# Kernel optimization log

Measured on AMD Instinct MI355X. Metric: run time of the kernel, lower is better.

The kernel has to match this reference:

```python
import jax, jax.numpy as jnp
import numpy as np

CUTOFF = 0.05

def _freq_filter(x_chw, filter_type):
    # x_chw: [C,H,W] = batch element 0, detached in the original (stop_gradient)
    x = jax.lax.stop_gradient(x_chw)
    C, H, W = x.shape
    a = jnp.abs(x)
    mn = a.min(axis=(1, 2), keepdims=True)
    ptp = a.max(axis=(1, 2), keepdims=True) - mn
    # np.uint8(255*(a-mn)/ptp): values in [0,255], cast truncates -> floor
    q = jnp.floor(255.0 * (a - mn) / ptp)
    f = jnp.fft.fftshift(jnp.fft.fft2(q), axes=(-2, -1))
    crow, ccol = H // 2, W // 2
    dr, dc = int(CUTOFF * crow), int(CUTOFF * ccol)
    m = jnp.zeros((H, W), dtype=q.dtype)
    m = m.at[crow - dr:crow + dr, ccol - dc:ccol + dc].set(1.0)
    if filter_type == 'low_pass':
        m = 1.0 - m  # note: original 'low_pass' actually removes low freqs
    out = jnp.abs(jnp.fft.ifft2(jnp.fft.ifftshift(f * m, axes=(-2, -1))))
    return out.astype(x_chw.dtype)  # [C,H,W]

def _conv1x1(x, w, b):
    # x: [B,C,H,W], w: [O,C], b: [O]
    return jnp.einsum('oc,bchw->bohw', w, x) + b[None, :, None, None]

def setup_inputs() -> dict:
    key = jax.random.key(0)
    ks = jax.random.split(key, 7)
    B, C, H, W = 1, 256, 96, 96
    fuse = jax.random.normal(ks[0], (B, C, H, W), dtype=jnp.float32)
    s = 1.0 / np.sqrt(C)
    Wq = jax.random.normal(ks[1], (C, C), dtype=jnp.float32) * s
    bq = jax.random.normal(ks[2], (C,), dtype=jnp.float32) * 0.01
    Wk = jax.random.normal(ks[3], (C, C), dtype=jnp.float32) * s
    bk = jax.random.normal(ks[4], (C,), dtype=jnp.float32) * 0.01
    Wv = jax.random.normal(ks[5], (C, C), dtype=jnp.float32) * s
    bv = jax.random.normal(ks[6], (C,), dtype=jnp.float32) * 0.01
    return {"fuse": fuse, "Wq": Wq, "bq": bq, "Wk": Wk, "bk": bk, "Wv": Wv, "bv": bv}

def reference(fuse, Wq, bq, Wk, bk, Wv, bv):
    B, C, H, W = fuse.shape
    scale = 1.0 / (C ** 0.5)
    # frequency-filtered maps (computed from batch 0, broadcast to all batches)
    FQ = jnp.broadcast_to(_freq_filter(fuse[0], 'high_pass'), fuse.shape)
    FK = jnp.broadcast_to(_freq_filter(fuse[0], 'low_pass'), fuse.shape)
    fuse_Query = _conv1x1(FQ, Wq, bq).reshape(B, C, H * W)     # [B,C,HW]
    fuse_Q_mask = fuse_Query.reshape(B * H, C * W)             # [B*H, C*W]
    fuse_Query_t = jnp.transpose(fuse_Query, (0, 2, 1))        # [B,HW,C]
    fuse_Key = _conv1x1(FK, Wk, bk).reshape(B, C, H * W)       # [B,C,HW]
    Fuse_Q_mask = jnp.max(fuse_Q_mask, axis=0, keepdims=True)  # [1, C*W]
    mask_KQ = jnp.einsum('bnc,bcm->bnm', fuse_Query_t, fuse_Key) * scale  # [B,HW,HW]
    mask_KQ = jax.nn.softmax(mask_KQ, axis=0)  # softmax over batch dim (as in original)
    mask_KQ = jnp.max(mask_KQ, axis=1)                         # [B,HW]
    mask_KQ = mask_KQ.reshape(-1, W)                           # [B*H, W]
    mask_KQ = jnp.max(mask_KQ, axis=-1, keepdims=True)         # [B*H, 1]
    mask = (mask_KQ @ Fuse_Q_mask).reshape(B, C, H, W)
    fuse_Value = _conv1x1(fuse, Wv, bv)
    return fuse_Value + fuse_Value * mask
```

## Files before the change

kernel.cpp:

```cpp
#include <hip/hip_runtime.h>
#include <math.h>

#define CCH 256
#define HW  9216
#define CW  24576
#define TWO_PI 6.28318530717958647692f

typedef __attribute__((ext_vector_type(8))) short short8;
typedef __attribute__((ext_vector_type(4))) float f32x4;

__device__ inline unsigned short f2bf(float f) {
    unsigned u = __float_as_uint(f);
    unsigned r = (u + 0x7FFFu + ((u >> 16) & 1u)) >> 16;
    return (unsigned short)r;
}

__global__ __launch_bounds__(768) void k_pre(const float* __restrict__ x,
                                             const float* __restrict__ Wq,
                                             const float* __restrict__ Wv,
                                             short8* __restrict__ Wqt,
                                             short8* __restrict__ Wvt,
                                             unsigned* __restrict__ FQm,
                                             float* __restrict__ Fg) {
    __shared__ float qa[HW];
    __shared__ float cs[96][2];
    __shared__ float Gp[8][96][5];
    __shared__ float Gs[96][6];
    __shared__ float red[24];
    __shared__ float s_mn, s_ptp;
    int bid = blockIdx.x, t = threadIdx.x;

    if (bid >= 256) {
        int widx = bid - 256;
        if (t < 256) {
            const float* src = (widx >= 32) ? Wv : Wq;
            short8* dst = (widx >= 32) ? Wvt : Wqt;
            int cidx = (widx & 31) * 256 + t;
            int ot = cidx >> 11, kc = (cidx >> 6) & 31, m = cidx & 63;
            const float* s = src + (ot * 64 + m) * 256 + kc * 8;
            short8 v;
            #pragma unroll
            for (int e = 0; e < 8; ++e) v[e] = (short)f2bf(s[e]);
            dst[cidx] = v;
        }
        return;
    }

    int c = bid;
    if (t < 96) FQm[c * 96 + t] = 0u;
    const float* xp = x + c * HW;
    if (t < 96) { float a = TWO_PI * (float)t / 96.0f; cs[t][0] = cosf(a); cs[t][1] = sinf(a); }
    float lo = 1e30f, hi = 0.f;
    #pragma unroll
    for (int i = 0; i < 12; ++i) {
        float a = fabsf(xp[t + i * 768]);
        qa[t + i * 768] = a;
        lo = fminf(lo, a);
        hi = fmaxf(hi, a);
    }
    #pragma unroll
    for (int d = 32; d; d >>= 1) {
        lo = fminf(lo, __shfl_xor(lo, d, 64));
        hi = fmaxf(hi, __shfl_xor(hi, d, 64));
    }
    if ((t & 63) == 0) { red[t >> 6] = lo; red[12 + (t >> 6)] = hi; }
    __syncthreads();
    if (t == 0) {
        lo = red[0]; hi = red[12];
        #pragma unroll
        for (int i = 1; i < 12; ++i) { lo = fminf(lo, red[i]); hi = fmaxf(hi, red[12 + i]); }
        s_mn = lo; s_ptp = hi - lo;
    }
    __syncthreads();
    float mn = s_mn, ptp = s_ptp;

    {
        int xx = t % 96, h = t / 96;
        float g0r = 0, g0i = 0, g1r = 0, g1i = 0, g2 = 0;
        for (int y = h * 12; y < h * 12 + 12; ++y) {
            float q = floorf(255.0f * (qa[y * 96 + xx] - mn) / ptp);
            float c1 = cs[y][0], s1 = cs[y][1];
            float c2 = c1 * c1 - s1 * s1, s2 = 2.0f * c1 * s1;
            g0r += q * c2; g0i += q * s2;
            g1r += q * c1; g1i += q * s1;
            g2  += q;
        }
        Gp[h][xx][0] = g0r; Gp[h][xx][1] = g0i;
        Gp[h][xx][2] = g1r; Gp[h][xx][3] = g1i;
        Gp[h][xx][4] = g2;
    }
    __syncthreads();
    if (t < 96) {
        #pragma unroll
        for (int j = 0; j < 5; ++j) {
            float s = 0.f;
            #pragma unroll
            for (int h = 0; h < 8; ++h) s += Gp[h][t][j];
            Gs[t][j] = s;
        }
        Gs[t][5] = 0.f;
    }
    __syncthreads();
    if (t < 64) {
        int coef = t >> 2, qq = t & 3;
        int ky = coef >> 2, kx = coef & 3;
        float fr = 0, fi = 0;
        for (int xx = qq * 24; xx < qq * 24 + 24; ++xx) {
            float c1 = cs[xx][0], s1 = cs[xx][1];
            float er, ei;
            if (kx == 0)      { er = c1 * c1 - s1 * s1; ei = 2.0f * c1 * s1; }
            else if (kx == 1) { er = c1; ei = s1; }
            else if (kx == 2) { er = 1.f; ei = 0.f; }
            else              { er = c1; ei = -s1; }
            float gr, gi;
            if (ky == 0)      { gr = Gs[xx][0]; gi = Gs[xx][1]; }
            else if (ky == 1) { gr = Gs[xx][2]; gi = Gs[xx][3]; }
            else if (ky == 2) { gr = Gs[xx][4]; gi = 0.f; }
            else              { gr = Gs[xx][2]; gi = -Gs[xx][3]; }
            fr += gr * er - gi * ei;
            fi += gr * ei + gi * er;
        }
        fr += __shfl_xor(fr, 1, 64); fr += __shfl_xor(fr, 2, 64);
        fi += __shfl_xor(fi, 1, 64); fi += __shfl_xor(fi, 2, 64);
        if (qq == 0) {
            Fg[c * 32 + 2 * coef]     = fr;
            Fg[c * 32 + 2 * coef + 1] = fi;
        }
    }
}

__global__ __launch_bounds__(256) void k_gemmQV(const short8* __restrict__ Wqt,
                                                const short8* __restrict__ Wvt,
                                                const float* __restrict__ Fg,
                                                const float* __restrict__ bq,
                                                const float* __restrict__ bv,
                                                const float* __restrict__ x,
                                                unsigned* __restrict__ FQm,
                                                float* __restrict__ out) {
    __shared__ short8 As[2048];
    __shared__ short8 Bs[2048];
    __shared__ float Rs[2048][2];
    float (*fq)[64] = (float (*)[64])Rs;
    int tid = threadIdx.x;
    int pt_ = blockIdx.x;
    bool isQ = blockIdx.y == 0;
    int p0 = pt_ * 64;

    int l = tid & 63, w = tid >> 6;
    int wr = w >> 1, wc = w & 1;
    int l15 = l & 15, quad = l >> 4;
    int abase = wr * 32 + l15;
    int bbase = wc * 32 + l15;

    if (isQ) {
        short8 areg[8];
        #pragma unroll
        for (int i = 0; i < 8; ++i) areg[i] = Wqt[i * 256 + tid];

        int y0 = p0 / 96;
        {
            int yi = (tid >> 2) & 1, kx = tid & 3, cb = tid >> 3;
            float ay = TWO_PI * (float)(y0 + yi) / 96.0f;
            float cyv = cosf(ay), syv = sinf(ay);
            float cy2 = cyv * cyv - syv * syv, sy2 = 2.f * cyv * syv;
            float Ur[4] = { cy2, cyv, 1.f, cyv };
            float Ui[4] = { -sy2, -syv, 0.f, syv };
            #pragma unroll
            for (int i = 0; i < 8; ++i) {
                int cc = cb + i * 32;
                float rr = 0.f, ri = 0.f;
                #pragma unroll
                for (int ky = 0; ky < 4; ++ky) {
                    float fr = Fg[cc * 32 + 2 * (ky * 4 + kx)];
                    float fi = Fg[cc * 32 + 2 * (ky * 4 + kx) + 1];
                    rr += fr * Ur[ky] - fi * Ui[ky];
                    ri += fr * Ui[ky] + fi * Ur[ky];
                }
                Rs[cc * 8 + yi * 4 + kx][0] = rr;
                Rs[cc * 8 + yi * 4 + kx][1] = ri;
            }
        }
        __syncthreads();
        const float inv = 1.0f / 9216.0f;
        #pragma unroll
        for (int i = 0; i < 8; ++i) {
            int si = i * 256 + tid;
            int kcg = si >> 6, n = si & 63;
            int p = p0 + n;
            int y = p / 96, xx = p - y * 96;
            int yi = y - y0;
            float axv = TWO_PI * (float)xx / 96.0f;
            float cxv = cosf(axv), sxv = sinf(axv);
            float cx2 = cxv * cxv - sxv * sxv, sx2 = 2.f * cxv * sxv;
            float Tr[4] = { cx2, cxv, 1.f, cxv };
            float Ti[4] = { -sx2, -sxv, 0.f, sxv };
            short8 vv;
            #pragma unroll
            for (int e = 0; e < 8; ++e) {
                int rb = (kcg * 8 + e) * 8 + yi * 4;
                float ar = 0.f, ai = 0.f;
                #pragma unroll
                for (int kx = 0; kx < 4; ++kx) {
                    float rr = Rs[rb + kx][0], ri = Rs[rb + kx][1];
                    ar += rr * Tr[kx] - ri * Ti[kx];
                    ai += rr * Ti[kx] + ri * Tr[kx];
                }
                vv[e] = (short)f2bf(sqrtf(ar * ar + ai * ai) * inv);
            }
            Bs[si] = vv;
        }
        __syncthreads();

        float vmax[2][4];
        #pragma unroll
        for (int ni = 0; ni < 2; ++ni)
            #pragma unroll
            for (int r = 0; r < 4; ++r) vmax[ni][r] = -3.0e38f;

        #pragma unroll
        for (int ot = 0; ot < 4; ++ot) {
            #pragma unroll
            for (int i = 0; i < 8; ++i) As[i * 256 + tid] = areg[i];
            __syncthreads();
            if (ot < 3) {
                #pragma unroll
                for (int i = 0; i < 8; ++i) areg[i] = Wqt[(ot + 1) * 2048 + i * 256 + tid];
            }
            f32x4 acc[2][2] = {};
            #pragma unroll
            for (int s = 0; s < 8; ++s) {
                int kc = s * 4 + quad;
                short8 a0 = As[kc * 64 + abase];
                short8 a1 = As[kc * 64 + abase + 16];
                short8 b0 = Bs[kc * 64 + bbase];
                short8 b1 = Bs[kc * 64 + bbase + 16];
                acc[0][0] = __builtin_amdgcn_mfma_f32_16x16x32_bf16(a0, b0, acc[0][0], 0, 0, 0);
                acc[0][1] = __builtin_amdgcn_mfma_f32_16x16x32_bf16(a0, b1, acc[0][1], 0, 0, 0);
                acc[1][0] = __builtin_amdgcn_mfma_f32_16x16x32_bf16(a1, b0, acc[1][0], 0, 0, 0);
                acc[1][1] = __builtin_amdgcn_mfma_f32_16x16x32_bf16(a1, b1, acc[1][1], 0, 0, 0);
            }
            #pragma unroll
            for (int ni = 0; ni < 2; ++ni) {
                #pragma unroll
                for (int r = 0; r < 4; ++r) {
                    int o_lo = ot * 64 + wr * 32 + quad * 4 + r;
                    float v = fmaxf(acc[0][ni][r] + bq[o_lo], acc[1][ni][r] + bq[o_lo + 16]);
                    vmax[ni][r] = fmaxf(vmax[ni][r], v);
                }
            }
            __syncthreads();
        }

        #pragma unroll
        for (int ni = 0; ni < 2; ++ni)
            #pragma unroll
            for (int r = 0; r < 4; ++r)
                vmax[ni][r] = fmaxf(vmax[ni][r], __shfl_xor(vmax[ni][r], 32, 64));
        if (wr == 0 && quad < 2) {
            #pragma unroll
            for (int ni = 0; ni < 2; ++ni)
                #pragma unroll
                for (int r = 0; r < 4; ++r)
                    fq[quad * 4 + r][wc * 32 + ni * 16 + l15] = vmax[ni][r];
        }
        __syncthreads();
        if (wr == 1 && quad < 2) {
            #pragma unroll
            for (int ni = 0; ni < 2; ++ni) {
                #pragma unroll
                for (int r = 0; r < 4; ++r) {
                    int row = quad * 4 + r;
                    int col = wc * 32 + ni * 16 + l15;
                    float v = fmaxf(vmax[ni][r], fq[row][col]);
                    int p = p0 + col;
                    int k = row * HW + p;
                    if (k >= CW) k -= CW;
                    if (k >= CW) k -= CW;
                    unsigned u = __float_as_uint(v);
                    unsigned key = (u & 0x80000000u) ? ~u : (u | 0x80000000u);
                    atomicMax(&FQm[k], key);
                }
            }
        }
        return;
    }

    int ot = blockIdx.y - 1;
    const short8* wsrc = Wvt + ot * 2048;
    #pragma unroll
    for (int i = 0; i < 8; ++i) As[i * 256 + tid] = wsrc[i * 256 + tid];

    #pragma unroll
    for (int i = 0; i < 8; ++i) {
        int si = i * 256 + tid;
        int KC = si >> 6, n = si & 63;
        const float* xb = x + (size_t)(KC * 8) * HW + p0 + n;
        short8 v;
        #pragma unroll
        for (int e = 0; e < 8; ++e) v[e] = (short)f2bf(xb[(size_t)e * HW]);
        Bs[si] = v;
    }
    __syncthreads();

    f32x4 acc[2][2] = {};
    #pragma unroll
    for (int s = 0; s < 8; ++s) {
        int kc = s * 4 + quad;
        short8 a0 = As[kc * 64 + abase];
        short8 a1 = As[kc * 64 + abase + 16];
        short8 b0 = Bs[kc * 64 + bbase];
        short8 b1 = Bs[kc * 64 + bbase + 16];
        acc[0][0] = __builtin_amdgcn_mfma_f32_16x16x32_bf16(a0, b0, acc[0][0], 0, 0, 0);
        acc[0][1] = __builtin_amdgcn_mfma_f32_16x16x32_bf16(a0, b1, acc[0][1], 0, 0, 0);
        acc[1][0] = __builtin_amdgcn_mfma_f32_16x16x32_bf16(a1, b0, acc[1][0], 0, 0, 0);
        acc[1][1] = __builtin_amdgcn_mfma_f32_16x16x32_bf16(a1, b1, acc[1][1], 0, 0, 0);
    }

    #pragma unroll
    for (int mi = 0; mi < 2; ++mi) {
        #pragma unroll
        for (int ni = 0; ni < 2; ++ni) {
            #pragma unroll
            for (int r = 0; r < 4; ++r) {
                int o = ot * 64 + wr * 32 + mi * 16 + quad * 4 + r;
                int p = p0 + wc * 32 + ni * 16 + l15;
                out[(size_t)o * HW + p] = acc[mi][ni][r] + bv[o];
            }
        }
    }
}

__device__ inline float mdecode(unsigned key) {
    unsigned ub = (key & 0x80000000u) ? (key ^ 0x80000000u) : ~key;
    return __uint_as_float(ub);
}
__global__ __launch_bounds__(256) void k_mask(float* __restrict__ out,
                                              const unsigned* __restrict__ FQm) {
    int i = (blockIdx.x * 256 + threadIdx.x) * 8;
    int o = i / HW;
    int p = i - o * HW;
    int k = (o & 7) * HW + p;
    if (k >= CW) k -= CW;
    if (k >= CW) k -= CW;
    float4 v0 = *(const float4*)(out + i);
    float4 v1 = *(const float4*)(out + i + 4);
    uint4 k0 = *(const uint4*)(FQm + k);
    uint4 k1 = *(const uint4*)(FQm + k + 4);
    v0.x *= 1.0f + mdecode(k0.x); v0.y *= 1.0f + mdecode(k0.y);
    v0.z *= 1.0f + mdecode(k0.z); v0.w *= 1.0f + mdecode(k0.w);
    v1.x *= 1.0f + mdecode(k1.x); v1.y *= 1.0f + mdecode(k1.y);
    v1.z *= 1.0f + mdecode(k1.z); v1.w *= 1.0f + mdecode(k1.w);
    *(float4*)(out + i)     = v0;
    *(float4*)(out + i + 4) = v1;
}

extern "C" void kernel_launch(void* const* d_in, const int* in_sizes, int n_in,
                              void* d_out, int out_size, void* d_ws, size_t ws_size,
                              hipStream_t stream) {
    const float* fuse = (const float*)d_in[0];
    const float* Wq   = (const float*)d_in[1];
    const float* bq   = (const float*)d_in[2];
    const float* Wv   = (const float*)d_in[5];
    const float* bv   = (const float*)d_in[6];
    float* out = (float*)d_out;

    char* ws = (char*)d_ws;
    unsigned* FQm = (unsigned*)(ws);
    float*    Fg  = (float*)(ws + 98304);
    short8*   Wqt = (short8*)(ws + 131072);
    short8*   Wvt = (short8*)(ws + 262144);

    k_pre<<<320, 768, 0, stream>>>(fuse, Wq, Wv, Wqt, Wvt, FQm, Fg);
    k_gemmQV<<<dim3(144, 5), 256, 0, stream>>>(Wqt, Wvt, Fg, bq, bv, fuse, FQm, out);
    k_mask<<<1152, 256, 0, stream>>>(out, FQm);
}
```

Measured before the change: 103.5 us.

## Split Q and V GEMMs, fuse mask multiply into V GEMM epilogue

Splits the combined Q/V GEMM kernel into a Q kernel that builds the mask and a separate V kernel that runs after it. The V kernel reads the finished mask and applies (1+mask) in its epilogue, so the separate elementwise mask pass and its full re-read and re-write of the output are removed. Each V block now computes two output tiles with fewer blocks (144x2), reusing the converted input tile. The cost is that the V GEMM can no longer overlap with the Q GEMM, since it now waits on a kernel boundary, and there is less parallelism in the V launch.

Measured after the change: 102.5 us. Within noise of the previous version (-0.9%).

```diff
diff --git a/kernel.cpp b/kernel.cpp
--- a/kernel.cpp
+++ b/kernel.cpp
@@ -129,21 +129,16 @@
     }
 }
 
-__global__ __launch_bounds__(256) void k_gemmQV(const short8* __restrict__ Wqt,
-                                                const short8* __restrict__ Wvt,
-                                                const float* __restrict__ Fg,
-                                                const float* __restrict__ bq,
-                                                const float* __restrict__ bv,
-                                                const float* __restrict__ x,
-                                                unsigned* __restrict__ FQm,
-                                                float* __restrict__ out) {
+__global__ __launch_bounds__(256) void k_gemmQ(const short8* __restrict__ Wqt,
+                                               const float* __restrict__ Fg,
+                                               const float* __restrict__ bq,
+                                               unsigned* __restrict__ FQm) {
     __shared__ short8 As[2048];
     __shared__ short8 Bs[2048];
     __shared__ float Rs[2048][2];
     float (*fq)[64] = (float (*)[64])Rs;
     int tid = threadIdx.x;
     int pt_ = blockIdx.x;
-    bool isQ = blockIdx.y == 0;
     int p0 = pt_ * 64;
 
     int l = tid & 63, w = tid >> 6;
@@ -152,143 +147,162 @@
     int abase = wr * 32 + l15;
     int bbase = wc * 32 + l15;
 
-    if (isQ) {
-        short8 areg[8];
-        #pragma unroll
-        for (int i = 0; i < 8; ++i) areg[i] = Wqt[i * 256 + tid];
-
-        int y0 = p0 / 96;
-        {
-            int yi = (tid >> 2) & 1, kx = tid & 3, cb = tid >> 3;
-            float ay = TWO_PI * (float)(y0 + yi) / 96.0f;
-            float cyv = cosf(ay), syv = sinf(ay);
-            float cy2 = cyv * cyv - syv * syv, sy2 = 2.f * cyv * syv;
-            float Ur[4] = { cy2, cyv, 1.f, cyv };
-            float Ui[4] = { -sy2, -syv, 0.f, syv };
-            #pragma unroll
-            for (int i = 0; i < 8; ++i) {
-                int cc = cb + i * 32;
-                float rr = 0.f, ri = 0.f;
-                #pragma unroll
-                for (int ky = 0; ky < 4; ++ky) {
-                    float fr = Fg[cc * 32 + 2 * (ky * 4 + kx)];
-                    float fi = Fg[cc * 32 + 2 * (ky * 4 + kx) + 1];
-                    rr += fr * Ur[ky] - fi * Ui[ky];
-                    ri += fr * Ui[ky] + fi * Ur[ky];
-                }
-                Rs[cc * 8 + yi * 4 + kx][0] = rr;
-                Rs[cc * 8 + yi * 4 + kx][1] = ri;
-            }
-        }
+    short8 areg[8];
+    #pragma unroll
+    for (int i = 0; i < 8; ++i) areg[i] = Wqt[i * 256 + tid];
+
+    int y0 = p0 / 96;
+    {
+        int yi = (tid >> 2) & 1, kx = tid & 3, cb = tid >> 3;
+        float ay = TWO_PI * (float)(y0 + yi) / 96.0f;
+        float cyv = cosf(ay), syv = sinf(ay);
+        float cy2 = cyv * cyv - syv * syv, sy2 = 2.f * cyv * syv;
+        float Ur[4] = { cy2, cyv, 1.f, cyv };
+        float Ui[4] = { -sy2, -syv, 0.f, syv };
+        #pragma unroll
+        for (int i = 0; i < 8; ++i) {
+            int cc = cb + i * 32;
+            float rr = 0.f, ri = 0.f;
+            #pragma unroll
+            for (int ky = 0; ky < 4; ++ky) {
+                float fr = Fg[cc * 32 + 2 * (ky * 4 + kx)];
+                float fi = Fg[cc * 32 + 2 * (ky * 4 + kx) + 1];
+                rr += fr * Ur[ky] - fi * Ui[ky];
+                ri += fr * Ui[ky] + fi * Ur[ky];
+            }
+            Rs[cc * 8 + yi * 4 + kx][0] = rr;
+            Rs[cc * 8 + yi * 4 + kx][1] = ri;
+        }
+    }
+    __syncthreads();
+    const float inv = 1.0f / 9216.0f;
+    #pragma unroll
+    for (int i = 0; i < 8; ++i) {
+        int si = i * 256 + tid;
+        int kcg = si >> 6, n = si & 63;
+        int p = p0 + n;
+        int y = p / 96, xx = p - y * 96;
+        int yi = y - y0;
+        float axv = TWO_PI * (float)xx / 96.0f;
+        float cxv = cosf(axv), sxv = sinf(axv);
+        float cx2 = cxv * cxv - sxv * sxv, sx2 = 2.f * cxv * sxv;
+        float Tr[4] = { cx2, cxv, 1.f, cxv };
+        float Ti[4] = { -sx2, -sxv, 0.f, sxv };
+        short8 vv;
+        #pragma unroll
+        for (int e = 0; e < 8; ++e) {
+            int rb = (kcg * 8 + e) * 8 + yi * 4;
+            float ar = 0.f, ai = 0.f;
+            #pragma unroll
+            for (int kx = 0; kx < 4; ++kx) {
+                float rr = Rs[rb + kx][0], ri = Rs[rb + kx][1];
+                ar += rr * Tr[kx] - ri * Ti[kx];
+                ai += rr * Ti[kx] + ri * Tr[kx];
+            }
+            vv[e] = (short)f2bf(sqrtf(ar * ar + ai * ai) * inv);
+        }
+        Bs[si] = vv;
+    }
+    __syncthreads();
+
+    float vmax[2][4];
+    #pragma unroll
+    for (int ni = 0; ni < 2; ++ni)
+        #pragma unroll
+        for (int r = 0; r < 4; ++r) vmax[ni][r] = -3.0e38f;
+
+    #pragma unroll
+    for (int ot = 0; ot < 4; ++ot) {
+        #pragma unroll
+        for (int i = 0; i < 8; ++i) As[i * 256 + tid] = areg[i];
         __syncthreads();
-        const float inv = 1.0f / 9216.0f;
-        #pragma unroll
-        for (int i = 0; i < 8; ++i) {
-            int si = i * 256 + tid;
-            int kcg = si >> 6, n = si & 63;
-            int p = p0 + n;
-            int y = p / 96, xx = p - y * 96;
-            int yi = y - y0;
-            float axv = TWO_PI * (float)xx / 96.0f;
-            float cxv = cosf(axv), sxv = sinf(axv);
-            float cx2 = cxv * cxv - sxv * sxv, sx2 = 2.f * cxv * sxv;
-            float Tr[4] = { cx2, cxv, 1.f, cxv };
-            float Ti[4] = { -sx2, -sxv, 0.f, sxv };
-            short8 vv;
-            #pragma unroll
-            for (int e = 0; e < 8; ++e) {
-                int rb = (kcg * 8 + e) * 8 + yi * 4;
-                float ar = 0.f, ai = 0.f;
-                #pragma unroll
-                for (int kx = 0; kx < 4; ++kx) {
-                    float rr = Rs[rb + kx][0], ri = Rs[rb + kx][1];
-                    ar += rr * Tr[kx] - ri * Ti[kx];
-                    ai += rr * Ti[kx] + ri * Tr[kx];
-                }
-                vv[e] = (short)f2bf(sqrtf(ar * ar + ai * ai) * inv);
-            }
-            Bs[si] = vv;
+        if (ot < 3) {
+            #pragma unroll
+            for (int i = 0; i < 8; ++i) areg[i] = Wqt[(ot + 1) * 2048 + i * 256 + tid];
+        }
+        f32x4 acc[2][2] = {};
+        #pragma unroll
+        for (int s = 0; s < 8; ++s) {
+            int kc = s * 4 + quad;
+            short8 a0 = As[kc * 64 + abase];
+            short8 a1 = As[kc * 64 + abase + 16];
+            short8 b0 = Bs[kc * 64 + bbase];
+            short8 b1 = Bs[kc * 64 + bbase + 16];
+            acc[0][0] = __builtin_amdgcn_mfma_f32_16x16x32_bf16(a0, b0, acc[0][0], 0, 0, 0);
+            acc[0][1] = __builtin_amdgcn_mfma_f32_16x16x32_bf16(a0, b1, acc[0][1], 0, 0, 0);
+            acc[1][0] = __builtin_amdgcn_mfma_f32_16x16x32_bf16(a1, b0, acc[1][0], 0, 0, 0);
+            acc[1][1] = __builtin_amdgcn_mfma_f32_16x16x32_bf16(a1, b1, acc[1][1], 0, 0, 0);
+        }
+        #pragma unroll
+        for (int ni = 0; ni < 2; ++ni) {
+            #pragma unroll
+            for (int r = 0; r < 4; ++r) {
+                int o_lo = ot * 64 + wr * 32 + quad * 4 + r;
+                float v = fmaxf(acc[0][ni][r] + bq[o_lo], acc[1][ni][r] + bq[o_lo + 16]);
+                vmax[ni][r] = fmaxf(vmax[ni][r], v);
+            }
         }
         __syncthreads();
-
-        float vmax[2][4];
+    }
+
+    #pragma unroll
+    for (int ni = 0; ni < 2; ++ni)
+        #pragma unroll
+        for (int r = 0; r < 4; ++r)
+            vmax[ni][r] = fmaxf(vmax[ni][r], __shfl_xor(vmax[ni][r], 32, 64));
+    if (wr == 0 && quad < 2) {
         #pragma unroll
         for (int ni = 0; ni < 2; ++ni)
             #pragma unroll
-            for (int r = 0; r < 4; ++r) vmax[ni][r] = -3.0e38f;
-
-        #pragma unroll
-        for (int ot = 0; ot < 4; ++ot) {
-            #pragma unroll
-            for (int i = 0; i < 8; ++i) As[i * 256 + tid] = areg[i];
-            __syncthreads();
-            if (ot < 3) {
-                #pragma unroll
-                for (int i = 0; i < 8; ++i) areg[i] = Wqt[(ot + 1) * 2048 + i * 256 + tid];
-            }
-            f32x4 acc[2][2] = {};
-            #pragma unroll
-            for (int s = 0; s < 8; ++s) {
-                int kc = s * 4 + quad;
-                short8 a0 = As[kc * 64 + abase];
-                short8 a1 = As[kc * 64 + abase + 16];
-                short8 b0 = Bs[kc * 64 + bbase];
-                short8 b1 = Bs[kc * 64 + bbase + 16];
-                acc[0][0] = __builtin_amdgcn_mfma_f32_16x16x32_bf16(a0, b0, acc[0][0], 0, 0, 0);
-                acc[0][1] = __builtin_amdgcn_mfma_f32_16x16x32_bf16(a0, b1, acc[0][1], 0, 0, 0);
-                acc[1][0] = __builtin_amdgcn_mfma_f32_16x16x32_bf16(a1, b0, acc[1][0], 0, 0, 0);
-                acc[1][1] = __builtin_amdgcn_mfma_f32_16x16x32_bf16(a1, b1, acc[1][1], 0, 0, 0);
-            }
-            #pragma unroll
-            for (int ni = 0; ni < 2; ++ni) {
-                #pragma unroll
-                for (int r = 0; r < 4; ++r) {
-                    int o_lo = ot * 64 + wr * 32 + quad * 4 + r;
-                    float v = fmaxf(acc[0][ni][r] + bq[o_lo], acc[1][ni][r] + bq[o_lo + 16]);
-                    vmax[ni][r] = fmaxf(vmax[ni][r], v);
-                }
-            }
-            __syncthreads();
-        }
-
-        #pragma unroll
-        for (int ni = 0; ni < 2; ++ni)
-            #pragma unroll
             for (int r = 0; r < 4; ++r)
-                vmax[ni][r] = fmaxf(vmax[ni][r], __shfl_xor(vmax[ni][r], 32, 64));
-        if (wr == 0 && quad < 2) {
-            #pragma unroll
-            for (int ni = 0; ni < 2; ++ni)
-                #pragma unroll
-                for (int r = 0; r < 4; ++r)
-                    fq[quad * 4 + r][wc * 32 + ni * 16 + l15] = vmax[ni][r];
-        }
-        __syncthreads();
-        if (wr == 1 && quad < 2) {
-            #pragma unroll
-            for (int ni = 0; ni < 2; ++ni) {
-                #pragma unroll
-                for (int r = 0; r < 4; ++r) {
-                    int row = quad * 4 + r;
-                    int col = wc * 32 + ni * 16 + l15;
-                    float v = fmaxf(vmax[ni][r], fq[row][col]);
-                    int p = p0 + col;
-                    int k = row * HW + p;
-                    if (k >= CW) k -= CW;
-                    if (k >= CW) k -= CW;
-                    unsigned u = __float_as_uint(v);
-                    unsigned key = (u & 0x80000000u) ? ~u : (u | 0x80000000u);
-                    atomicMax(&FQm[k], key);
-                }
-            }
-        }
-        return;
-    }
-
-    int ot = blockIdx.y - 1;
-    const short8* wsrc = Wvt + ot * 2048;
-    #pragma unroll
-    for (int i = 0; i < 8; ++i) As[i * 256 + tid] = wsrc[i * 256 + tid];
+                fq[quad * 4 + r][wc * 32 + ni * 16 + l15] = vmax[ni][r];
+    }
+    __syncthreads();
+    if (wr == 1 && quad < 2) {
+        #pragma unroll
+        for (int ni = 0; ni < 2; ++ni) {
+            #pragma unroll
+            for (int r = 0; r < 4; ++r) {
+                int row = quad * 4 + r;
+                int col = wc * 32 + ni * 16 + l15;
+                float v = fmaxf(vmax[ni][r], fq[row][col]);
+                int p = p0 + col;
+                int k = row * HW + p;
+                if (k >= CW) k -= CW;
+                if (k >= CW) k -= CW;
+                unsigned u = __float_as_uint(v);
+                unsigned key = (u & 0x80000000u) ? ~u : (u | 0x80000000u);
+                atomicMax(&FQm[k], key);
+            }
+        }
+    }
+}
+
+__device__ inline float mdecode(unsigned key) {
+    unsigned ub = (key & 0x80000000u) ? (key ^ 0x80000000u) : ~key;
+    return __uint_as_float(ub);
+}
+__global__ __launch_bounds__(256) void k_gemmV(const short8* __restrict__ Wvt,
+                                               const float* __restrict__ bv,
+                                               const float* __restrict__ x,
+                                               const unsigned* __restrict__ FQm,
+                                               float* __restrict__ out) {
+    __shared__ short8 As[2048];
+    __shared__ short8 Bs[2048];
+    int tid = threadIdx.x;
+    int pt_ = blockIdx.x;
+    int yv = blockIdx.y;
+    int p0 = pt_ * 64;
+
+    int l = tid & 63, w = tid >> 6;
+    int wr = w >> 1, wc = w & 1;
+    int l15 = l & 15, quad = l >> 4;
+    int abase = wr * 32 + l15;
+    int bbase = wc * 32 + l15;
+
+    short8 areg[8];
+    #pragma unroll
+    for (int i = 0; i < 8; ++i) areg[i] = Wvt[(yv * 2) * 2048 + i * 256 + tid];
 
     #pragma unroll
     for (int i = 0; i < 8; ++i) {
@@ -300,58 +314,58 @@
         for (int e = 0; e < 8; ++e) v[e] = (short)f2bf(xb[(size_t)e * HW]);
         Bs[si] = v;
     }
-    __syncthreads();
-
-    f32x4 acc[2][2] = {};
-    #pragma unroll
-    for (int s = 0; s < 8; ++s) {
-        int kc = s * 4 + quad;
-        short8 a0 = As[kc * 64 + abase];
-        short8 a1 = As[kc * 64 + abase + 16];
-        short8 b0 = Bs[kc * 64 + bbase];
-        short8 b1 = Bs[kc * 64 + bbase + 16];
-        acc[0][0] = __builtin_amdgcn_mfma_f32_16x16x32_bf16(a0, b0, acc[0][0], 0, 0, 0);
-        acc[0][1] = __builtin_amdgcn_mfma_f32_16x16x32_bf16(a0, b1, acc[0][1], 0, 0, 0);
-        acc[1][0] = __builtin_amdgcn_mfma_f32_16x16x32_bf16(a1, b0, acc[1][0], 0, 0, 0);
-        acc[1][1] = __builtin_amdgcn_mfma_f32_16x16x32_bf16(a1, b1, acc[1][1], 0, 0, 0);
-    }
-
-    #pragma unroll
-    for (int mi = 0; mi < 2; ++mi) {
-        #pragma unroll
-        for (int ni = 0; ni < 2; ++ni) {
-            #pragma unroll
-            for (int r = 0; r < 4; ++r) {
-                int o = ot * 64 + wr * 32 + mi * 16 + quad * 4 + r;
-                int p = p0 + wc * 32 + ni * 16 + l15;
-                out[(size_t)o * HW + p] = acc[mi][ni][r] + bv[o];
-            }
-        }
-    }
-}
-
-__device__ inline float mdecode(unsigned key) {
-    unsigned ub = (key & 0x80000000u) ? (key ^ 0x80000000u) : ~key;
-    return __uint_as_float(ub);
-}
-__global__ __launch_bounds__(256) void k_mask(float* __restrict__ out,
-                                              const unsigned* __restrict__ FQm) {
-    int i = (blockIdx.x * 256 + threadIdx.x) * 8;
-    int o = i / HW;
-    int p = i - o * HW;
-    int k = (o & 7) * HW + p;
-    if (k >= CW) k -= CW;
-    if (k >= CW) k -= CW;
-    float4 v0 = *(const float4*)(out + i);
-    float4 v1 = *(const float4*)(out + i + 4);
-    uint4 k0 = *(const uint4*)(FQm + k);
-    uint4 k1 = *(const uint4*)(FQm + k + 4);
-    v0.x *= 1.0f + mdecode(k0.x); v0.y *= 1.0f + mdecode(k0.y);
-    v0.z *= 1.0f + mdecode(k0.z); v0.w *= 1.0f + mdecode(k0.w);
-    v1.x *= 1.0f + mdecode(k1.x); v1.y *= 1.0f + mdecode(k1.y);
-    v1.z *= 1.0f + mdecode(k1.z); v1.w *= 1.0f + mdecode(k1.w);
-    *(float4*)(out + i)     = v0;
-    *(float4*)(out + i + 4) = v1;
+
+    float msk[2][4];
+    #pragma unroll
+    for (int ni = 0; ni < 2; ++ni) {
+        #pragma unroll
+        for (int r = 0; r < 4; ++r) {
+            int row = (quad * 4 + r) & 7;
+            int p = p0 + wc * 32 + ni * 16 + l15;
+            int k = row * HW + p;
+            if (k >= CW) k -= CW;
+            if (k >= CW) k -= CW;
+            msk[ni][r] = mdecode(FQm[k]);
+        }
+    }
+
+    #pragma unroll
+    for (int j = 0; j < 2; ++j) {
+        int ot = yv * 2 + j;
+        #pragma unroll
+        for (int i = 0; i < 8; ++i) As[i * 256 + tid] = areg[i];
+        __syncthreads();
+        if (j == 0) {
+            #pragma unroll
+            for (int i = 0; i < 8; ++i) areg[i] = Wvt[(yv * 2 + 1) * 2048 + i * 256 + tid];
+        }
+        f32x4 acc[2][2] = {};
+        #pragma unroll
+        for (int s = 0; s < 8; ++s) {
+            int kc = s * 4 + quad;
+            short8 a0 = As[kc * 64 + abase];
+            short8 a1 = As[kc * 64 + abase + 16];
+            short8 b0 = Bs[kc * 64 + bbase];
+            short8 b1 = Bs[kc * 64 + bbase + 16];
+            acc[0][0] = __builtin_amdgcn_mfma_f32_16x16x32_bf16(a0, b0, acc[0][0], 0, 0, 0);
+            acc[0][1] = __builtin_amdgcn_mfma_f32_16x16x32_bf16(a0, b1, acc[0][1], 0, 0, 0);
+            acc[1][0] = __builtin_amdgcn_mfma_f32_16x16x32_bf16(a1, b0, acc[1][0], 0, 0, 0);
+            acc[1][1] = __builtin_amdgcn_mfma_f32_16x16x32_bf16(a1, b1, acc[1][1], 0, 0, 0);
+        }
+        #pragma unroll
+        for (int mi = 0; mi < 2; ++mi) {
+            #pragma unroll
+            for (int ni = 0; ni < 2; ++ni) {
+                #pragma unroll
+                for (int r = 0; r < 4; ++r) {
+                    int o = ot * 64 + wr * 32 + mi * 16 + quad * 4 + r;
+                    int p = p0 + wc * 32 + ni * 16 + l15;
+                    out[(size_t)o * HW + p] = (acc[mi][ni][r] + bv[o]) * (1.0f + msk[ni][r]);
+                }
+            }
+        }
+        __syncthreads();
+    }
 }
 
 extern "C" void kernel_launch(void* const* d_in, const int* in_sizes, int n_in,
@@ -371,6 +385,6 @@
     short8*   Wvt = (short8*)(ws + 262144);
 
     k_pre<<<320, 768, 0, stream>>>(fuse, Wq, Wv, Wqt, Wvt, FQm, Fg);
-    k_gemmQV<<<dim3(144, 5), 256, 0, stream>>>(Wqt, Wvt, Fg, bq, bv, fuse, FQm, out);
-    k_mask<<<1152, 256, 0, stream>>>(out, FQm);
-}
+    k_gemmQ<<<144, 256, 0, stream>>>(Wqt, Fg, bq, FQm);
+    k_gemmV<<<dim3(144, 2), 256, 0, stream>>>(Wvt, bv, fuse, FQm, out);
+}
```
